# Optimization experiments

Hardware: AMD Instinct MI355X
Metric: run time of the kernel (lower is better)

Reference implementation:

```python
import jax, jax.numpy as jnp
import numpy as np

N = 50000
E = 300000
ATOM_DIM = 128
HID = 256
NODE_DIM = 64
NUM_LAYERS = 3
G = 2000  # number of graphs
LN_EPS = 1e-5


def setup_inputs() -> dict:
    key = jax.random.key(0)
    ks = jax.random.split(key, 12)
    x = jax.random.normal(ks[0], (N, ATOM_DIM), dtype=jnp.float32)
    edge_index = jax.random.randint(ks[1], (2, E), 0, N, dtype=jnp.int64)
    batch = jnp.sort(jax.random.randint(ks[2], (N,), 0, G, dtype=jnp.int64))
    s = 1.0 / np.sqrt(HID)
    W_enc = jax.random.normal(ks[3], (ATOM_DIM, HID), dtype=jnp.float32) * (1.0 / np.sqrt(ATOM_DIM))
    b_enc = jnp.zeros((HID,), dtype=jnp.float32)
    Ws = jax.random.normal(ks[4], (NUM_LAYERS, HID, HID), dtype=jnp.float32) * s
    bs = jnp.zeros((NUM_LAYERS, HID), dtype=jnp.float32)
    Wp = jax.random.normal(ks[5], (HID, NODE_DIM), dtype=jnp.float32) * s
    bp = jnp.zeros((NODE_DIM,), dtype=jnp.float32)
    gamma = jnp.ones((NODE_DIM,), dtype=jnp.float32)
    beta = jnp.zeros((NODE_DIM,), dtype=jnp.float32)
    return {"x": x, "edge_index": edge_index, "batch": batch,
            "W_enc": W_enc, "b_enc": b_enc, "Ws": Ws, "bs": bs,
            "Wp": Wp, "bp": bp, "gamma": gamma, "beta": beta}


def _gcn_conv(h, src, dst, dinv_src_dst, W, b):
    # h: [N, H]; PyG GCNConv: (D^-1/2 (A+I) D^-1/2) (h W) + b
    hw = h @ W                                      # [N, H]
    msg = hw[src] * dinv_src_dst[:, None]           # [E+N, H] gather + scale
    agg = jnp.zeros_like(hw).at[dst].add(msg)       # scatter-add to dst
    return agg + b


def reference(x, edge_index, batch, W_enc, b_enc, Ws, bs, Wp, bp, gamma, beta):
    n = x.shape[0]
    # add self loops (GCNConv default)
    loops = jnp.arange(n, dtype=edge_index.dtype)
    src = jnp.concatenate([edge_index[0], loops])
    dst = jnp.concatenate([edge_index[1], loops])
    # symmetric degree normalization computed on dst (PyG convention)
    deg = jax.ops.segment_sum(jnp.ones_like(dst, dtype=x.dtype), dst, num_segments=n)
    dinv = jnp.where(deg > 0, jax.lax.rsqrt(deg), 0.0)
    norm = dinv[src] * dinv[dst]                    # [E+N]

    h = x @ W_enc + b_enc                           # atom encoder
    for i in range(NUM_LAYERS):
        h = jax.nn.relu(_gcn_conv(h, src, dst, norm, Ws[i], bs[i]))
        # dropout is identity in eval mode

    # global_mean_pool over graph ids
    sums = jax.ops.segment_sum(h, batch, num_segments=G)          # [G, H]
    cnts = jax.ops.segment_sum(jnp.ones((n,), dtype=h.dtype), batch, num_segments=G)
    mol = sums / jnp.maximum(cnts, 1.0)[:, None]

    # projection: Linear -> LayerNorm
    p = mol @ Wp + bp                                # [G, NODE_DIM]
    mu = jnp.mean(p, axis=-1, keepdims=True)
    var = jnp.mean((p - mu) ** 2, axis=-1, keepdims=True)
    return (p - mu) * jax.lax.rsqrt(var + LN_EPS) * gamma + beta
```

## Files before the change

### kernel.cpp

```cpp
#include <hip/hip_runtime.h>
#include <hip/hip_bf16.h>

#define NN 50000
#define EE 300000
#define ATOM_DIM 128
#define HID 256
#define NODE_DIM 64
#define NUM_LAYERS 3
#define GG 2000
#define LN_EPS 1e-5f
#define CSRC_CAP 704512

typedef __attribute__((ext_vector_type(8))) short bf16x8;
typedef __attribute__((ext_vector_type(4))) float f32x4;

__device__ __forceinline__ ushort f2bf(float f) {
    __hip_bfloat16 h = __float2bfloat16(f);
    return *reinterpret_cast<ushort*>(&h);
}
__device__ __forceinline__ float bf2f(ushort u) {
    __hip_bfloat16 h = *reinterpret_cast<__hip_bfloat16*>(&u);
    return __bfloat162float(h);
}

__device__ __forceinline__ void gll16(const void* g, void* l) {
    __builtin_amdgcn_global_load_lds((const __attribute__((address_space(1))) unsigned int*)g,
                                     (__attribute__((address_space(3))) unsigned int*)l, 16, 0, 0);
}


#define PB_CVT   6250
#define PB_WTE   32
#define PB_WTL   192
#define PB_GB    8
#define PB_CSRC  688
#define PB_CNT   49
#define PB_ZROW  1
#define PB_TOTAL (PB_CVT + PB_WTE + PB_WTL + PB_GB + PB_CSRC + PB_CNT + PB_ZROW)

__device__ __forceinline__ void wt_tile(const float* __restrict__ W, ushort* __restrict__ Wt,
                                        int K, int N, int bx, int by) {
    __shared__ float t[32][33];
    int lx = threadIdx.x & 31, ly = threadIdx.x >> 5;
#pragma unroll
    for (int s = 0; s < 32; s += 8)
        t[ly + s][lx] = W[(size_t)(by * 32 + ly + s) * N + bx * 32 + lx];
    __syncthreads();
#pragma unroll
    for (int s = 0; s < 32; s += 8)
        Wt[(size_t)(bx * 32 + ly + s) * K + by * 32 + lx] = f2bf(t[lx][ly + s]);
}

__global__ __launch_bounds__(256) void k_prep(const float* __restrict__ x, ushort* __restrict__ xbf,
                                              const float* __restrict__ W_enc, ushort* __restrict__ wtE,
                                              const float* __restrict__ Ws, ushort* __restrict__ wtL,
                                              const int* __restrict__ batch, int* __restrict__ gstart,
                                              int* __restrict__ cnt, int* __restrict__ csrc,
                                              ushort* __restrict__ hbf_zero_row) {
    int b = blockIdx.x;
    int tid = threadIdx.x;
    if (b < PB_CVT) {
        int i = (b * 256 + tid) * 4;
        float4 v = *(const float4*)&x[i];
        ushort4 o;
        o.x = f2bf(v.x); o.y = f2bf(v.y); o.z = f2bf(v.z); o.w = f2bf(v.w);
        *(ushort4*)&xbf[i] = o;
        return;
    }
    b -= PB_CVT;
    if (b < PB_WTE) {
        wt_tile(W_enc, wtE, ATOM_DIM, HID, b & 7, b >> 3);
        return;
    }
    b -= PB_WTE;
    if (b < PB_WTL) {
        int z = b >> 6, r = b & 63;
        wt_tile(Ws + (size_t)z * HID * HID, wtL + (size_t)z * HID * HID, HID, HID, r & 7, r >> 3);
        return;
    }
    b -= PB_WTL;
    if (b < PB_GB) {
        int g = b * 256 + tid;
        if (g > GG) return;
        int lo = 0, hi = NN;
        while (lo < hi) { int mid = (lo + hi) >> 1; if (batch[mid] < g) lo = mid + 1; else hi = mid; }
        gstart[g] = lo;
        return;
    }
    b -= PB_GB;
    if (b < PB_CSRC) {
        int i = (b * 256 + tid) * 4;
        if (i < CSRC_CAP) *(int4*)&csrc[i] = make_int4(NN, NN, NN, NN);
        return;
    }
    b -= PB_CSRC;
    if (b < PB_CNT) {
        int i = (b * 256 + tid) * 4;
        if (i < NN) *(int4*)&cnt[i] = make_int4(0, 0, 0, 0);
        return;
    }
    hbf_zero_row[tid] = 0;
}


__global__ __launch_bounds__(256) void k_count(const int* __restrict__ ei, int* cnt, int e_total) {
    int e = blockIdx.x * 256 + threadIdx.x;
    if (e < e_total) atomicAdd(&cnt[ei[e_total + e]], 1);
}

__global__ __launch_bounds__(256) void k_scan1(const int* __restrict__ cnt, int* __restrict__ rowp,
                                               int* __restrict__ csum, int n) {
    __shared__ int s[256];
    int tid = threadIdx.x;
    int base = blockIdx.x * 1024 + tid * 4;
    int v[4];
#pragma unroll
    for (int j = 0; j < 4; ++j) { int i = base + j; v[j] = (i < n) ? ((cnt[i] + 8) & ~7) : 0; }
    int tsum = v[0] + v[1] + v[2] + v[3];
    s[tid] = tsum;
    __syncthreads();
    for (int off = 1; off < 256; off <<= 1) {
        int t = (tid >= off) ? s[tid - off] : 0;
        __syncthreads();
        s[tid] += t;
        __syncthreads();
    }
    int excl = s[tid] - tsum;
#pragma unroll
    for (int j = 0; j < 4; ++j) { int i = base + j; if (i < n) rowp[i] = excl; excl += v[j]; }
    if (tid == 255) csum[blockIdx.x] = s[255];
}

__global__ __launch_bounds__(256) void k_scan2(int* __restrict__ rowp, int* __restrict__ fill,
                                               const int* __restrict__ csum, const int* __restrict__ cnt,
                                               float* __restrict__ dinv, int n) {
    __shared__ int soff;
    int chunk = blockIdx.x;
    if (threadIdx.x == 0) {
        int o = 0;
        for (int c = 0; c < chunk; ++c) o += csum[c];
        soff = o;
    }
    __syncthreads();
    int off = soff;
    int base = chunk * 1024 + threadIdx.x * 4;
#pragma unroll
    for (int j = 0; j < 4; ++j) {
        int i = base + j;
        if (i < n) {
            int r = rowp[i] + off;
            rowp[i] = r; fill[i] = r;
            dinv[i] = rsqrtf((float)(cnt[i] + 1));
        }
    }
    if (chunk == gridDim.x - 1 && threadIdx.x == 255) rowp[n] = off + csum[chunk];
}

__global__ __launch_bounds__(256) void k_fill(const int* __restrict__ ei, int* fill, int* __restrict__ csrc,
                                              int e_total, int n) {
    int e = blockIdx.x * 256 + threadIdx.x;
    int tot = e_total + n;
    if (e >= tot) return;
    int s, d;
    if (e < e_total) { s = ei[e]; d = ei[e_total + e]; }
    else { s = d = e - e_total; }
    int pos = atomicAdd(&fill[d], 1);
    csrc[pos] = s;
}


__global__ __launch_bounds__(256) void k_gemm_bf16(const ushort* __restrict__ A, const ushort* __restrict__ Bt,
                                                   const float* __restrict__ bias, ushort* __restrict__ Cb,
                                                   const float* __restrict__ dscale, int relu,
                                                   int M, int K, int NC) {
    __shared__ short As[4096];
    __shared__ short Bs[4096];
    int tid = threadIdx.x;
    int lane = tid & 63, w = tid >> 6;
    int wr = w >> 1, wc = w & 1;
    int row0 = blockIdx.x * 128, col0 = blockIdx.y * 128;

    f32x4 acc[4][4] = {};

    int r15 = lane & 15;
    int swz = ((r15 >> 1) & 3) << 3;
    int kseg = (lane >> 4) << 3;
    int koff = kseg ^ swz;

    int st_row[2], st_cg[2];
#pragma unroll
    for (int i = 0; i < 2; ++i) {
        int row = i * 64 + (tid >> 2);
        st_row[i] = row;
        st_cg[i] = (tid & 3) ^ ((row >> 1) & 3);
    }

    for (int k0 = 0; k0 < K; k0 += 32) {
#pragma unroll
        for (int i = 0; i < 2; ++i) {
            int ra = row0 + st_row[i];
            if (ra > M - 1) ra = M - 1;
            gll16(A + (size_t)ra * K + k0 + st_cg[i] * 8, &As[i * 2048 + w * 512]);
            gll16(Bt + (size_t)(col0 + st_row[i]) * K + k0 + st_cg[i] * 8, &Bs[i * 2048 + w * 512]);
        }
        __syncthreads();
        bf16x8 af[4], bfr[4];
#pragma unroll
        for (int m = 0; m < 4; ++m) af[m] = *(const bf16x8*)&As[(wr * 64 + m * 16 + r15) * 32 + koff];
#pragma unroll
        for (int n = 0; n < 4; ++n) bfr[n] = *(const bf16x8*)&Bs[(wc * 64 + n * 16 + r15) * 32 + koff];
#pragma unroll
        for (int m = 0; m < 4; ++m)
#pragma unroll
            for (int n = 0; n < 4; ++n)
                acc[m][n] = __builtin_amdgcn_mfma_f32_16x16x32_bf16(af[m], bfr[n], acc[m][n], 0, 0, 0);
        __syncthreads();
    }

    int cc = lane & 15, rq = (lane >> 4) * 4;
#pragma unroll
    for (int m = 0; m < 4; ++m) {
#pragma unroll
        for (int r = 0; r < 4; ++r) {
            int gr = row0 + wr * 64 + m * 16 + rq + r;
            if (gr >= M) continue;
            float ds = dscale ? dscale[gr] : 1.0f;
#pragma unroll
            for (int n = 0; n < 4; ++n) {
                int gc = col0 + wc * 64 + n * 16 + cc;
                float v = acc[m][n][r];
                if (bias) v += bias[gc];
                if (relu) v = fmaxf(v, 0.f);
                Cb[(size_t)gr * NC + gc] = f2bf(v * ds);
            }
        }
    }
}


__global__ __launch_bounds__(256) void k_aggregate_bf(const ushort* __restrict__ hin,
                                                      const int* __restrict__ rowp,
                                                      const int* __restrict__ csrc,
                                                      const float* __restrict__ dinv,
                                                      ushort* __restrict__ aout, int n) {
    int wave = threadIdx.x >> 6, lane = threadIdx.x & 63;
    int node = blockIdx.x * 4 + wave;
    if (node >= n) return;
    int beg = __builtin_amdgcn_readfirstlane(rowp[node]);
    int end = __builtin_amdgcn_readfirstlane(rowp[node + 1]);
    const ushort* hc = hin + lane * 4;
    float4 acc = make_float4(0.f, 0.f, 0.f, 0.f);
    for (int j = beg; j < end; j += 8) {
        int s0 = csrc[j + 0], s1 = csrc[j + 1], s2 = csrc[j + 2], s3 = csrc[j + 3];
        int s4 = csrc[j + 4], s5 = csrc[j + 5], s6 = csrc[j + 6], s7 = csrc[j + 7];
        ushort4 r0 = *(const ushort4*)&hc[(size_t)s0 * HID];
        ushort4 r1 = *(const ushort4*)&hc[(size_t)s1 * HID];
        ushort4 r2 = *(const ushort4*)&hc[(size_t)s2 * HID];
        ushort4 r3 = *(const ushort4*)&hc[(size_t)s3 * HID];
        ushort4 r4 = *(const ushort4*)&hc[(size_t)s4 * HID];
        ushort4 r5 = *(const ushort4*)&hc[(size_t)s5 * HID];
        ushort4 r6 = *(const ushort4*)&hc[(size_t)s6 * HID];
        ushort4 r7 = *(const ushort4*)&hc[(size_t)s7 * HID];
        acc.x += ((bf2f(r0.x) + bf2f(r1.x)) + (bf2f(r2.x) + bf2f(r3.x))) +
                 ((bf2f(r4.x) + bf2f(r5.x)) + (bf2f(r6.x) + bf2f(r7.x)));
        acc.y += ((bf2f(r0.y) + bf2f(r1.y)) + (bf2f(r2.y) + bf2f(r3.y))) +
                 ((bf2f(r4.y) + bf2f(r5.y)) + (bf2f(r6.y) + bf2f(r7.y)));
        acc.z += ((bf2f(r0.z) + bf2f(r1.z)) + (bf2f(r2.z) + bf2f(r3.z))) +
                 ((bf2f(r4.z) + bf2f(r5.z)) + (bf2f(r6.z) + bf2f(r7.z)));
        acc.w += ((bf2f(r0.w) + bf2f(r1.w)) + (bf2f(r2.w) + bf2f(r3.w))) +
                 ((bf2f(r4.w) + bf2f(r5.w)) + (bf2f(r6.w) + bf2f(r7.w)));
    }
    float dn = dinv[node];
    ushort4 o;
    o.x = f2bf(dn * acc.x); o.y = f2bf(dn * acc.y);
    o.z = f2bf(dn * acc.z); o.w = f2bf(dn * acc.w);
    *(ushort4*)&aout[(size_t)node * HID + lane * 4] = o;
}


__global__ __launch_bounds__(256) void k_pool_proj_ln(const ushort* __restrict__ hbf, const int* __restrict__ gstart,
                                                      const float* __restrict__ Wp, const float* __restrict__ bp,
                                                      const float* __restrict__ gamma, const float* __restrict__ beta,
                                                      float* __restrict__ out) {
    __shared__ float mol[HID];
    __shared__ float part[4][NODE_DIM];
    int g = blockIdx.x;
    int t = threadIdx.x;
    int beg = gstart[g], end = gstart[g + 1];
    float sum = 0.f;
    for (int r = beg; r < end; ++r) sum += bf2f(hbf[(size_t)r * HID + t]);
    float inv = 1.0f / fmaxf((float)(end - beg), 1.0f);
    mol[t] = sum * inv;
    __syncthreads();
    int w = t >> 6, j = t & 63;
    float p = 0.f;
    int k0 = w * 64;
#pragma unroll 8
    for (int k = 0; k < 64; ++k) p += mol[k0 + k] * Wp[(size_t)(k0 + k) * NODE_DIM + j];
    part[w][j] = p;
    __syncthreads();
    if (t < 64) {
        float pj = part[0][j] + part[1][j] + part[2][j] + part[3][j] + bp[j];
        float s = pj;
#pragma unroll
        for (int m = 1; m < 64; m <<= 1) s += __shfl_xor(s, m);
        float mu = s * (1.0f / 64.0f);
        float d = pj - mu;
        float vs = d * d;
#pragma unroll
        for (int m = 1; m < 64; m <<= 1) vs += __shfl_xor(vs, m);
        out[(size_t)g * NODE_DIM + j] = d * rsqrtf(vs * (1.0f / 64.0f) + LN_EPS) * gamma[j] + beta[j];
    }
}


extern "C" void kernel_launch(void* const* d_in, const int* in_sizes, int n_in,
                              void* d_out, int out_size, void* d_ws, size_t ws_size,
                              hipStream_t stream) {
    const float* x     = (const float*)d_in[0];
    const int*   ei    = (const int*)d_in[1];
    const int*   batch = (const int*)d_in[2];
    const float* W_enc = (const float*)d_in[3];
    const float* b_enc = (const float*)d_in[4];
    const float* Ws    = (const float*)d_in[5];
    const float* bs    = (const float*)d_in[6];
    const float* Wp    = (const float*)d_in[7];
    const float* bp    = (const float*)d_in[8];
    const float* gamma = (const float*)d_in[9];
    const float* beta  = (const float*)d_in[10];
    float* out = (float*)d_out;

    ushort* hbf  = (ushort*)d_ws;
    ushort* abf  = hbf + (size_t)(NN + 1) * HID;
    ushort* xbf  = abf + (size_t)NN * HID;
    ushort* wtE  = xbf + (size_t)NN * ATOM_DIM;
    ushort* wtL  = wtE + HID * ATOM_DIM;
    float*  dinv = (float*)(wtL + (size_t)NUM_LAYERS * HID * HID);
    int* cnt    = (int*)(dinv + NN);
    int* rowp   = cnt + NN;
    int* fill   = rowp + NN + 1;
    int* csrc   = fill + NN;
    int* csum   = csrc + CSRC_CAP;
    int* gstart = csum + 64;

    const int EN = EE + NN;
    const int NCH = (NN + 1023) / 1024;

    k_prep<<<PB_TOTAL, 256, 0, stream>>>(x, xbf, W_enc, wtE, Ws, wtL, batch, gstart,
                                         cnt, csrc, hbf + (size_t)NN * HID);

    k_count<<<(EE + 255) / 256, 256, 0, stream>>>(ei, cnt, EE);
    k_scan1<<<NCH, 256, 0, stream>>>(cnt, rowp, csum, NN);
    k_scan2<<<NCH, 256, 0, stream>>>(rowp, fill, csum, cnt, dinv, NN);
    k_fill<<<(EN + 255) / 256, 256, 0, stream>>>(ei, fill, csrc, EE, NN);

    dim3 ggrid((NN + 127) / 128, HID / 128);

    k_gemm_bf16<<<ggrid, 256, 0, stream>>>(xbf, wtE, b_enc, hbf, dinv, 0, NN, ATOM_DIM, HID);

    for (int l = 0; l < NUM_LAYERS; ++l) {
        k_aggregate_bf<<<(NN + 3) / 4, 256, 0, stream>>>(hbf, rowp, csrc, dinv, abf, NN);
        const float* ds = (l < NUM_LAYERS - 1) ? dinv : nullptr;
        k_gemm_bf16<<<ggrid, 256, 0, stream>>>(abf, wtL + (size_t)l * HID * HID, bs + (size_t)l * HID,
                                               hbf, ds, 1, NN, HID, HID);
    }

    k_pool_proj_ln<<<GG, 256, 0, stream>>>(hbf, gstart, Wp, bp, gamma, beta, out);
}
```

Before: 305.2 us.

## Double-buffer GEMM LDS tiles and swap grid axes for column-adjacent blocks

The bf16 MFMA GEMM now uses two LDS buffers, so the global-to-LDS loads for the next K-slice are issued before the current slice is computed. This takes one barrier out of each K iteration. The grid is also transposed so the two column blocks that share a row tile launch next to each other, which should improve L2 reuse of the A rows. The cost is twice the LDS footprint, which could lower occupancy.

```diff
diff --git a/kernel.cpp b/kernel.cpp
--- a/kernel.cpp
+++ b/kernel.cpp
@@ -173,49 +173,66 @@
                                                    const float* __restrict__ bias, ushort* __restrict__ Cb,
                                                    const float* __restrict__ dscale, int relu,
                                                    int M, int K, int NC) {
-    __shared__ short As[4096];
-    __shared__ short Bs[4096];
+    __shared__ short As[2][4096];
+    __shared__ short Bs[2][4096];
     int tid = threadIdx.x;
     int lane = tid & 63, w = tid >> 6;
     int wr = w >> 1, wc = w & 1;
-    int row0 = blockIdx.x * 128, col0 = blockIdx.y * 128;
+    int row0 = blockIdx.y * 128, col0 = blockIdx.x * 128;
 
     f32x4 acc[4][4] = {};
 
     int r15 = lane & 15;
     int swz = ((r15 >> 1) & 3) << 3;
-    int kseg = (lane >> 4) << 3;
-    int koff = kseg ^ swz;
-
-    int st_row[2], st_cg[2];
+    int koff = ((lane >> 4) << 3) ^ swz;
+
+    const ushort* aB[2];
+    const ushort* bB[2];
 #pragma unroll
     for (int i = 0; i < 2; ++i) {
         int row = i * 64 + (tid >> 2);
-        st_row[i] = row;
-        st_cg[i] = (tid & 3) ^ ((row >> 1) & 3);
-    }
-
-    for (int k0 = 0; k0 < K; k0 += 32) {
-#pragma unroll
-        for (int i = 0; i < 2; ++i) {
-            int ra = row0 + st_row[i];
-            if (ra > M - 1) ra = M - 1;
-            gll16(A + (size_t)ra * K + k0 + st_cg[i] * 8, &As[i * 2048 + w * 512]);
-            gll16(Bt + (size_t)(col0 + st_row[i]) * K + k0 + st_cg[i] * 8, &Bs[i * 2048 + w * 512]);
-        }
+        int cg = (tid & 3) ^ ((row >> 1) & 3);
+        int ra = row0 + row; if (ra > M - 1) ra = M - 1;
+        aB[i] = A + (size_t)ra * K + cg * 8;
+        bB[i] = Bt + (size_t)(col0 + row) * K + cg * 8;
+    }
+    int ldst = w * 512;
+
+#define STAGE(buf, kk) do { int k0_ = (kk) << 5;                      \
+        gll16(aB[0] + k0_, &As[buf][ldst]);                           \
+        gll16(aB[1] + k0_, &As[buf][2048 + ldst]);                    \
+        gll16(bB[0] + k0_, &Bs[buf][ldst]);                           \
+        gll16(bB[1] + k0_, &Bs[buf][2048 + ldst]);                    \
+    } while (0)
+
+#define COMPUTE(buf) do {                                                              \
+        bf16x8 af[4], bfr[4];                                                          \
+        _Pragma("unroll")                                                              \
+        for (int m = 0; m < 4; ++m)                                                    \
+            af[m] = *(const bf16x8*)&As[buf][(wr * 64 + m * 16 + r15) * 32 + koff];    \
+        _Pragma("unroll")                                                              \
+        for (int n = 0; n < 4; ++n)                                                    \
+            bfr[n] = *(const bf16x8*)&Bs[buf][(wc * 64 + n * 16 + r15) * 32 + koff];   \
+        _Pragma("unroll")                                                              \
+        for (int m = 0; m < 4; ++m)                                                    \
+            _Pragma("unroll")                                                          \
+            for (int n = 0; n < 4; ++n)                                                \
+                acc[m][n] = __builtin_amdgcn_mfma_f32_16x16x32_bf16(af[m], bfr[n], acc[m][n], 0, 0, 0); \
+    } while (0)
+
+    int nk = K >> 5;
+    STAGE(0, 0);
+    __syncthreads();
+    for (int t = 0; t < nk - 1; ++t) {
+        int buf = t & 1;
+        STAGE(buf ^ 1, t + 1);
+        COMPUTE(buf);
         __syncthreads();
-        bf16x8 af[4], bfr[4];
-#pragma unroll
-        for (int m = 0; m < 4; ++m) af[m] = *(const bf16x8*)&As[(wr * 64 + m * 16 + r15) * 32 + koff];
-#pragma unroll
-        for (int n = 0; n < 4; ++n) bfr[n] = *(const bf16x8*)&Bs[(wc * 64 + n * 16 + r15) * 32 + koff];
-#pragma unroll
-        for (int m = 0; m < 4; ++m)
-#pragma unroll
-            for (int n = 0; n < 4; ++n)
-                acc[m][n] = __builtin_amdgcn_mfma_f32_16x16x32_bf16(af[m], bfr[n], acc[m][n], 0, 0, 0);
-        __syncthreads();
-    }
+    }
+    COMPUTE((nk - 1) & 1);
+
+#undef STAGE
+#undef COMPUTE
 
     int cc = lane & 15, rq = (lane >> 4) * 4;
 #pragma unroll
@@ -354,7 +371,7 @@
     k_scan2<<<NCH, 256, 0, stream>>>(rowp, fill, csum, cnt, dinv, NN);
     k_fill<<<(EN + 255) / 256, 256, 0, stream>>>(ei, fill, csrc, EE, NN);
 
-    dim3 ggrid((NN + 127) / 128, HID / 128);
+    dim3 ggrid(HID / 128, (NN + 127) / 128);
 
     k_gemm_bf16<<<ggrid, 256, 0, stream>>>(xbf, wtE, b_enc, hbf, dinv, 0, NN, ATOM_DIM, HID);
 
```

Result: faster. 298.6 us (-2.2%).

## Replace LDS-staged GEMM with direct global-to-register MFMA GEMM

Applied to the files above, without the earlier changes.

The node GEMMs no longer stage A and B tiles through shared memory with barriers. Each wave now loads its MFMA fragments straight from global memory. Each block covers 64 rows across the full 256 output columns, and each wave owns 64 columns. K is a template parameter so the k-loop fully unrolls. This removes LDS traffic and __syncthreads, but each wave now reads its A rows separately, so A is fetched four times per block (presumably served by L1/L2). The per-lane global loads are 16-byte strided reads rather than coalesced tiles.

```diff
diff --git a/kernel.cpp b/kernel.cpp
--- a/kernel.cpp
+++ b/kernel.cpp
@@ -21,11 +21,6 @@
 __device__ __forceinline__ float bf2f(ushort u) {
     __hip_bfloat16 h = *reinterpret_cast<__hip_bfloat16*>(&u);
     return __bfloat162float(h);
-}
-
-__device__ __forceinline__ void gll16(const void* g, void* l) {
-    __builtin_amdgcn_global_load_lds((const __attribute__((address_space(1))) unsigned int*)g,
-                                     (__attribute__((address_space(3))) unsigned int*)l, 16, 0, 0);
 }
 
 
@@ -169,52 +164,45 @@
 }
 
 
-__global__ __launch_bounds__(256) void k_gemm_bf16(const ushort* __restrict__ A, const ushort* __restrict__ Bt,
-                                                   const float* __restrict__ bias, ushort* __restrict__ Cb,
-                                                   const float* __restrict__ dscale, int relu,
-                                                   int M, int K, int NC) {
-    __shared__ short As[4096];
-    __shared__ short Bs[4096];
+template <int K>
+__global__ __launch_bounds__(256) void k_gemm_direct(const ushort* __restrict__ A,
+                                                     const ushort* __restrict__ Bt,
+                                                     const float* __restrict__ bias,
+                                                     ushort* __restrict__ Cb,
+                                                     const float* __restrict__ dscale, int relu,
+                                                     int M) {
     int tid = threadIdx.x;
     int lane = tid & 63, w = tid >> 6;
-    int wr = w >> 1, wc = w & 1;
-    int row0 = blockIdx.x * 128, col0 = blockIdx.y * 128;
+    int row0 = blockIdx.x * 64;
+    int col0 = w * 64;
+    int r15 = lane & 15;
+    int kofs = (lane >> 4) * 8;
+
+    const ushort* aP[4];
+    const ushort* bP[4];
+#pragma unroll
+    for (int m = 0; m < 4; ++m) {
+        int r = row0 + m * 16 + r15; if (r > M - 1) r = M - 1;
+        aP[m] = A + (size_t)r * K + kofs;
+    }
+#pragma unroll
+    for (int n = 0; n < 4; ++n) {
+        bP[n] = Bt + (size_t)(col0 + n * 16 + r15) * K + kofs;
+    }
 
     f32x4 acc[4][4] = {};
-
-    int r15 = lane & 15;
-    int swz = ((r15 >> 1) & 3) << 3;
-    int kseg = (lane >> 4) << 3;
-    int koff = kseg ^ swz;
-
-    int st_row[2], st_cg[2];
-#pragma unroll
-    for (int i = 0; i < 2; ++i) {
-        int row = i * 64 + (tid >> 2);
-        st_row[i] = row;
-        st_cg[i] = (tid & 3) ^ ((row >> 1) & 3);
-    }
-
-    for (int k0 = 0; k0 < K; k0 += 32) {
-#pragma unroll
-        for (int i = 0; i < 2; ++i) {
-            int ra = row0 + st_row[i];
-            if (ra > M - 1) ra = M - 1;
-            gll16(A + (size_t)ra * K + k0 + st_cg[i] * 8, &As[i * 2048 + w * 512]);
-            gll16(Bt + (size_t)(col0 + st_row[i]) * K + k0 + st_cg[i] * 8, &Bs[i * 2048 + w * 512]);
-        }
-        __syncthreads();
+#pragma unroll
+    for (int t = 0; t < K / 32; ++t) {
         bf16x8 af[4], bfr[4];
 #pragma unroll
-        for (int m = 0; m < 4; ++m) af[m] = *(const bf16x8*)&As[(wr * 64 + m * 16 + r15) * 32 + koff];
-#pragma unroll
-        for (int n = 0; n < 4; ++n) bfr[n] = *(const bf16x8*)&Bs[(wc * 64 + n * 16 + r15) * 32 + koff];
+        for (int m = 0; m < 4; ++m) af[m] = *(const bf16x8*)(aP[m] + t * 32);
+#pragma unroll
+        for (int n = 0; n < 4; ++n) bfr[n] = *(const bf16x8*)(bP[n] + t * 32);
 #pragma unroll
         for (int m = 0; m < 4; ++m)
 #pragma unroll
             for (int n = 0; n < 4; ++n)
                 acc[m][n] = __builtin_amdgcn_mfma_f32_16x16x32_bf16(af[m], bfr[n], acc[m][n], 0, 0, 0);
-        __syncthreads();
     }
 
     int cc = lane & 15, rq = (lane >> 4) * 4;
@@ -222,16 +210,16 @@
     for (int m = 0; m < 4; ++m) {
 #pragma unroll
         for (int r = 0; r < 4; ++r) {
-            int gr = row0 + wr * 64 + m * 16 + rq + r;
+            int gr = row0 + m * 16 + rq + r;
             if (gr >= M) continue;
             float ds = dscale ? dscale[gr] : 1.0f;
 #pragma unroll
             for (int n = 0; n < 4; ++n) {
-                int gc = col0 + wc * 64 + n * 16 + cc;
+                int gc = col0 + n * 16 + cc;
                 float v = acc[m][n][r];
                 if (bias) v += bias[gc];
                 if (relu) v = fmaxf(v, 0.f);
-                Cb[(size_t)gr * NC + gc] = f2bf(v * ds);
+                Cb[(size_t)gr * HID + gc] = f2bf(v * ds);
             }
         }
     }
@@ -354,15 +342,15 @@
     k_scan2<<<NCH, 256, 0, stream>>>(rowp, fill, csum, cnt, dinv, NN);
     k_fill<<<(EN + 255) / 256, 256, 0, stream>>>(ei, fill, csrc, EE, NN);
 
-    dim3 ggrid((NN + 127) / 128, HID / 128);
-
-    k_gemm_bf16<<<ggrid, 256, 0, stream>>>(xbf, wtE, b_enc, hbf, dinv, 0, NN, ATOM_DIM, HID);
+    const int gblocks = (NN + 63) / 64;
+
+    k_gemm_direct<ATOM_DIM><<<gblocks, 256, 0, stream>>>(xbf, wtE, b_enc, hbf, dinv, 0, NN);
 
     for (int l = 0; l < NUM_LAYERS; ++l) {
         k_aggregate_bf<<<(NN + 3) / 4, 256, 0, stream>>>(hbf, rowp, csrc, dinv, abf, NN);
         const float* ds = (l < NUM_LAYERS - 1) ? dinv : nullptr;
-        k_gemm_bf16<<<ggrid, 256, 0, stream>>>(abf, wtL + (size_t)l * HID * HID, bs + (size_t)l * HID,
-                                               hbf, ds, 1, NN, HID, HID);
+        k_gemm_direct<HID><<<gblocks, 256, 0, stream>>>(abf, wtL + (size_t)l * HID * HID,
+                                                        bs + (size_t)l * HID, hbf, ds, 1, NN);
     }
 
     k_pool_proj_ln<<<GG, 256, 0, stream>>>(hbf, gstart, Wp, bp, gamma, beta, out);
```

Measured after the change: 358.5 us. +17.5%, slower.
